# Optimization experiments

Measured on AMD Instinct MI355X. Metric: run time of the kernel, lower is better.

Reference implementation:

```python
import jax, jax.numpy as jnp
import numpy as np

KERNEL_SIZE = 5
SIGMA_INTENSITY = 0.1
SIGMA_SPATIAL = 1.0
EPS = 1e-8


def make_spatial_kernel():
    coords = jnp.arange(KERNEL_SIZE, dtype=jnp.float32) - KERNEL_SIZE // 2
    x, y = jnp.meshgrid(coords, coords, indexing='ij')
    return jnp.exp(-(x ** 2 + y ** 2) / (2.0 * SIGMA_SPATIAL ** 2))


def setup_inputs() -> dict:
    key = jax.random.key(0)
    images = jax.random.uniform(key, (16, 3, 512, 512), dtype=jnp.float32)
    spatial_kernel = make_spatial_kernel()
    return {"images": images, "spatial_kernel": spatial_kernel}


def reference(images, spatial_kernel):
    B, C, H, W = images.shape
    K = KERNEL_SIZE
    p = K // 2
    # reflect pad (torch 'reflect' == jnp 'reflect', edge not repeated)
    padded = jnp.pad(images, ((0, 0), (0, 0), (p, p), (p, p)), mode='reflect')
    # extract K*K shifted views -> (B, C, K*K, H, W); fixed small loop over offsets
    patches = jnp.stack(
        [padded[:, :, i:i + H, j:j + W] for i in range(K) for j in range(K)],
        axis=2,
    )
    center_idx = K * K // 2
    center = patches[:, :, center_idx:center_idx + 1, :, :]
    diff = patches - center
    intensity_w = jnp.exp(-(diff ** 2) / (2.0 * SIGMA_INTENSITY ** 2))
    spatial_flat = spatial_kernel.reshape(1, 1, K * K, 1, 1)
    w = spatial_flat * intensity_w
    w = w / (jnp.sum(w, axis=2, keepdims=True) + EPS)
    filtered = jnp.sum(patches * w, axis=2)  # (B, C, H, W)
    return filtered
```

## Files before the change

kernel.cpp:

```cpp
#include <hip/hip_runtime.h>

#define IMG  512
#define TW   64
#define TH   8
#define HALO 2
#define LWD  68
#define LW   69
#define LH   12

typedef float v2f __attribute__((ext_vector_type(2)));
typedef int   v2i __attribute__((ext_vector_type(2)));

#define KS2      24598.990f
#define INV_KS2  4.0652061e-05f

__device__ __forceinline__ int reflect_idx(int g) {
    int a = abs(g);
    return min(a, 2 * IMG - 2 - a);
}

__global__ __launch_bounds__(256) void bilateral_kernel(
    const float* __restrict__ img, float* __restrict__ out)
{
    __shared__ float q[LH][LW];

    const int plane = blockIdx.z;
    const int x0 = blockIdx.x * TW;
    const int y0 = blockIdx.y * TH;
    const float* __restrict__ src = img + (size_t)plane * (IMG * IMG);

    const int tid = threadIdx.x + threadIdx.y * 32;

    #pragma unroll
    for (int i = 0; i < 4; ++i) {
        int idx = tid + i * 256;
        if (idx < LH * LWD) {
            int r = idx / LWD;
            int c = idx - r * LWD;
            q[r][c] = src[reflect_idx(y0 - HALO + r) * IMG + reflect_idx(x0 - HALO + c)] * KS2;
        }
    }
    __syncthreads();

    const int tx = threadIdx.x, ty = threadIdx.y;
    const float* bp = &q[ty][2 * tx];

    v2f qc;
    qc.x = bp[2 * LW + 2];
    qc.y = bp[2 * LW + 3];

    v2f wsum = {1.0f, 1.0f};
    v2f acc  = qc;

    #pragma unroll
    for (int dy = 0; dy < 5; ++dy) {
        #pragma unroll
        for (int dx = 0; dx < 5; ++dx) {
            if (dx == 2 && dy == 2) continue;
            const int r2 = (dx - 2) * (dx - 2) + (dy - 2) * (dy - 2);
            const float Ktap = (float)(1065353216.0 - 6051101.63118 * (double)r2);

            const int off = dy * LW + dx;
            v2f qt;
            qt.x = bp[off];
            qt.y = bp[off + 1];

            v2f d = qt - qc;
            v2f t = Ktap - d * d;
            v2i iv = __builtin_convertvector(t, v2i);
            v2f e = __builtin_bit_cast(v2f, iv);

            wsum += e;
            acc  += e * qt;
        }
    }

    v2f res;
    res.x = acc.x * __builtin_amdgcn_rcpf(wsum.x) * INV_KS2;
    res.y = acc.y * __builtin_amdgcn_rcpf(wsum.y) * INV_KS2;

    float* dst = out + (size_t)plane * (IMG * IMG)
                     + (size_t)(y0 + ty) * IMG + (x0 + 2 * tx);
    *reinterpret_cast<v2f*>(dst) = res;
}

extern "C" void kernel_launch(void* const* d_in, const int* in_sizes, int n_in,
                              void* d_out, int out_size, void* d_ws, size_t ws_size,
                              hipStream_t stream) {
    const float* img = (const float*)d_in[0];
    float* out = (float*)d_out;
    int planes = in_sizes[0] / (IMG * IMG);
    dim3 grid(IMG / TW, IMG / TH, planes);
    dim3 block(32, 8, 1);
    bilateral_kernel<<<grid, block, 0, stream>>>(img, out);
}
```

Before: 131.1 us.

## Enlarge tile and compute 2x4 pixels per thread with register window

The tile grows to 128x16 and each thread now produces a 2-wide by 4-tall output patch. It loads an 8x6 window of the shared tile into registers once, so neighbouring output rows reuse those values instead of re-reading LDS for every tap. The halo load becomes row-structured, using 64-wide threads per row, which removes the per-element divide and modulo. The aim is to cut LDS traffic and halo overhead per output. The cost is more registers per thread and fewer blocks in flight.

```diff
diff --git a/kernel.cpp b/kernel.cpp
--- a/kernel.cpp
+++ b/kernel.cpp
@@ -1,12 +1,15 @@
 #include <hip/hip_runtime.h>
 
 #define IMG  512
-#define TW   64
-#define TH   8
+#define BTX  64
+#define BTY  4
+#define PXY  4
+#define TW   128
+#define TH   16
 #define HALO 2
-#define LWD  68
-#define LW   69
-#define LH   12
+#define LWD  (TW + 4)
+#define LW   136
+#define LH   (TH + 4)
 
 typedef float v2f __attribute__((ext_vector_type(2)));
 typedef int   v2i __attribute__((ext_vector_type(2)));
@@ -29,59 +32,70 @@
     const int y0 = blockIdx.y * TH;
     const float* __restrict__ src = img + (size_t)plane * (IMG * IMG);
 
-    const int tid = threadIdx.x + threadIdx.y * 32;
+    const int tx = threadIdx.x, ty = threadIdx.y;
 
     #pragma unroll
-    for (int i = 0; i < 4; ++i) {
-        int idx = tid + i * 256;
-        if (idx < LH * LWD) {
-            int r = idx / LWD;
-            int c = idx - r * LWD;
-            q[r][c] = src[reflect_idx(y0 - HALO + r) * IMG + reflect_idx(x0 - HALO + c)] * KS2;
-        }
+    for (int p = 0; p < 5; ++p) {
+        int r  = 4 * p + ty;
+        int gr = reflect_idx(y0 - HALO + r) * IMG;
+        q[r][tx]      = src[gr + reflect_idx(x0 - HALO + tx)]      * KS2;
+        q[r][tx + 64] = src[gr + reflect_idx(x0 - HALO + tx + 64)] * KS2;
+        if (tx < 4)
+            q[r][tx + 128] = src[gr + reflect_idx(x0 - HALO + tx + 128)] * KS2;
     }
     __syncthreads();
 
-    const int tx = threadIdx.x, ty = threadIdx.y;
-    const float* bp = &q[ty][2 * tx];
-
-    v2f qc;
-    qc.x = bp[2 * LW + 2];
-    qc.y = bp[2 * LW + 3];
-
-    v2f wsum = {1.0f, 1.0f};
-    v2f acc  = qc;
-
+    float w[PXY + 4][6];
     #pragma unroll
-    for (int dy = 0; dy < 5; ++dy) {
-        #pragma unroll
-        for (int dx = 0; dx < 5; ++dx) {
-            if (dx == 2 && dy == 2) continue;
-            const int r2 = (dx - 2) * (dx - 2) + (dy - 2) * (dy - 2);
-            const float Ktap = (float)(1065353216.0 - 6051101.63118 * (double)r2);
-
-            const int off = dy * LW + dx;
-            v2f qt;
-            qt.x = bp[off];
-            qt.y = bp[off + 1];
-
-            v2f d = qt - qc;
-            v2f t = Ktap - d * d;
-            v2i iv = __builtin_convertvector(t, v2i);
-            v2f e = __builtin_bit_cast(v2f, iv);
-
-            wsum += e;
-            acc  += e * qt;
-        }
+    for (int r = 0; r < PXY + 4; ++r) {
+        const float* row = &q[PXY * ty + r][2 * tx];
+        v2f a = *reinterpret_cast<const v2f*>(row);
+        v2f b = *reinterpret_cast<const v2f*>(row + 2);
+        v2f c = *reinterpret_cast<const v2f*>(row + 4);
+        w[r][0] = a.x; w[r][1] = a.y;
+        w[r][2] = b.x; w[r][3] = b.y;
+        w[r][4] = c.x; w[r][5] = c.y;
     }
 
-    v2f res;
-    res.x = acc.x * __builtin_amdgcn_rcpf(wsum.x) * INV_KS2;
-    res.y = acc.y * __builtin_amdgcn_rcpf(wsum.y) * INV_KS2;
+    v2f res[PXY];
+    #pragma unroll
+    for (int p = 0; p < PXY; ++p) {
+        v2f qc;
+        qc.x = w[p + 2][2];
+        qc.y = w[p + 2][3];
+        v2f wsum = {1.0f, 1.0f};
+        v2f acc  = qc;
+
+        #pragma unroll
+        for (int dy = 0; dy < 5; ++dy) {
+            #pragma unroll
+            for (int dx = 0; dx < 5; ++dx) {
+                if (dx == 2 && dy == 2) continue;
+                const int r2 = (dx - 2) * (dx - 2) + (dy - 2) * (dy - 2);
+                const float Ktap = (float)(1065353216.0 - 6051101.63118 * (double)r2);
+
+                v2f qt;
+                qt.x = w[p + dy][dx];
+                qt.y = w[p + dy][dx + 1];
+
+                v2f d = qt - qc;
+                v2f t = Ktap - d * d;
+                v2i iv = __builtin_convertvector(t, v2i);
+                v2f e  = __builtin_bit_cast(v2f, iv);
+
+                wsum += e;
+                acc  += e * qt;
+            }
+        }
+        res[p].x = acc.x * __builtin_amdgcn_rcpf(wsum.x) * INV_KS2;
+        res[p].y = acc.y * __builtin_amdgcn_rcpf(wsum.y) * INV_KS2;
+    }
 
     float* dst = out + (size_t)plane * (IMG * IMG)
-                     + (size_t)(y0 + ty) * IMG + (x0 + 2 * tx);
-    *reinterpret_cast<v2f*>(dst) = res;
+                     + (size_t)(y0 + PXY * ty) * IMG + (x0 + 2 * tx);
+    #pragma unroll
+    for (int p = 0; p < PXY; ++p)
+        *reinterpret_cast<v2f*>(dst + p * IMG) = res[p];
 }
 
 extern "C" void kernel_launch(void* const* d_in, const int* in_sizes, int n_in,
@@ -91,6 +105,6 @@
     float* out = (float*)d_out;
     int planes = in_sizes[0] / (IMG * IMG);
     dim3 grid(IMG / TW, IMG / TH, planes);
-    dim3 block(32, 8, 1);
+    dim3 block(BTX, BTY, 1);
     bilateral_kernel<<<grid, block, 0, stream>>>(img, out);
 }
```

Result: no change. 132.3 us (+0.9%).

## Use 64x16 tiles with row-strided per-thread outputs and scalar taps

Applied to the files above, without the earlier changes.

Reshapes the tile from 64x8 to 64x16 with 64x4 thread blocks, so each thread computes four outputs spaced four rows apart instead of two horizontally adjacent pixels. This cuts halo overhead per output and replaces the generic index-divide halo load with a row-structured load. The packed v2f math becomes scalar fmaf code. The shared tile has no padding column (LW 68), which may cause bank conflicts. The grid shrinks, so fewer blocks are available to hide latency.

```diff
diff --git a/kernel.cpp b/kernel.cpp
--- a/kernel.cpp
+++ b/kernel.cpp
@@ -1,18 +1,14 @@
 #include <hip/hip_runtime.h>
+#include <stdint.h>
 
-#define IMG  512
-#define TW   64
-#define TH   8
-#define HALO 2
-#define LWD  68
-#define LW   69
-#define LH   12
+#define IMG 512
+#define KS2     24598.990f
+#define INV_KS2 4.0652061e-05f
 
-typedef float v2f __attribute__((ext_vector_type(2)));
-typedef int   v2i __attribute__((ext_vector_type(2)));
-
-#define KS2      24598.990f
-#define INV_KS2  4.0652061e-05f
+#define TW 64
+#define TH 16
+#define LW 68
+#define LH 20
 
 __device__ __forceinline__ int reflect_idx(int g) {
     int a = abs(g);
@@ -29,59 +25,45 @@
     const int y0 = blockIdx.y * TH;
     const float* __restrict__ src = img + (size_t)plane * (IMG * IMG);
 
-    const int tid = threadIdx.x + threadIdx.y * 32;
+    const int tx = threadIdx.x, ty = threadIdx.y;
 
     #pragma unroll
-    for (int i = 0; i < 4; ++i) {
-        int idx = tid + i * 256;
-        if (idx < LH * LWD) {
-            int r = idx / LWD;
-            int c = idx - r * LWD;
-            q[r][c] = src[reflect_idx(y0 - HALO + r) * IMG + reflect_idx(x0 - HALO + c)] * KS2;
-        }
+    for (int p = 0; p < 5; ++p) {
+        int r  = ty + 4 * p;
+        int gr = reflect_idx(y0 - 2 + r) * IMG;
+        q[r][tx] = src[gr + reflect_idx(x0 - 2 + tx)] * KS2;
+        if (tx < 4)
+            q[r][tx + 64] = src[gr + reflect_idx(x0 - 2 + tx + 64)] * KS2;
     }
     __syncthreads();
 
-    const int tx = threadIdx.x, ty = threadIdx.y;
-    const float* bp = &q[ty][2 * tx];
-
-    v2f qc;
-    qc.x = bp[2 * LW + 2];
-    qc.y = bp[2 * LW + 3];
-
-    v2f wsum = {1.0f, 1.0f};
-    v2f acc  = qc;
+    float* dst = out + (size_t)plane * (IMG * IMG)
+                     + (size_t)(y0 + ty) * IMG + (x0 + tx);
 
     #pragma unroll
-    for (int dy = 0; dy < 5; ++dy) {
+    for (int k = 0; k < 4; ++k) {
+        const int row = ty + 4 * k;
+        const float qc = q[row + 2][tx + 2];
+        float wsum = 1.0f;
+        float acc  = qc;
+
         #pragma unroll
-        for (int dx = 0; dx < 5; ++dx) {
-            if (dx == 2 && dy == 2) continue;
-            const int r2 = (dx - 2) * (dx - 2) + (dy - 2) * (dy - 2);
-            const float Ktap = (float)(1065353216.0 - 6051101.63118 * (double)r2);
-
-            const int off = dy * LW + dx;
-            v2f qt;
-            qt.x = bp[off];
-            qt.y = bp[off + 1];
-
-            v2f d = qt - qc;
-            v2f t = Ktap - d * d;
-            v2i iv = __builtin_convertvector(t, v2i);
-            v2f e = __builtin_bit_cast(v2f, iv);
-
-            wsum += e;
-            acc  += e * qt;
+        for (int dy = 0; dy < 5; ++dy) {
+            #pragma unroll
+            for (int dx = 0; dx < 5; ++dx) {
+                if (dy == 2 && dx == 2) continue;
+                const int r2 = (dx - 2) * (dx - 2) + (dy - 2) * (dy - 2);
+                const float Kf = (float)(1065353216.0 - 6051101.63118 * (double)r2);
+                const float qt = q[row + dy][tx + dx];
+                const float d  = qt - qc;
+                const float t  = __builtin_fmaf(-d, d, Kf);
+                const float e  = __builtin_bit_cast(float, (int)t);
+                wsum += e;
+                acc  = __builtin_fmaf(e, qt, acc);
+            }
         }
+        dst[(size_t)(4 * k) * IMG] = acc * __builtin_amdgcn_rcpf(wsum) * INV_KS2;
     }
-
-    v2f res;
-    res.x = acc.x * __builtin_amdgcn_rcpf(wsum.x) * INV_KS2;
-    res.y = acc.y * __builtin_amdgcn_rcpf(wsum.y) * INV_KS2;
-
-    float* dst = out + (size_t)plane * (IMG * IMG)
-                     + (size_t)(y0 + ty) * IMG + (x0 + 2 * tx);
-    *reinterpret_cast<v2f*>(dst) = res;
 }
 
 extern "C" void kernel_launch(void* const* d_in, const int* in_sizes, int n_in,
@@ -89,8 +71,9 @@
                               hipStream_t stream) {
     const float* img = (const float*)d_in[0];
     float* out = (float*)d_out;
-    int planes = in_sizes[0] / (IMG * IMG);
+    const int planes = in_sizes[0] / (IMG * IMG);
+
     dim3 grid(IMG / TW, IMG / TH, planes);
-    dim3 block(32, 8, 1);
+    dim3 block(64, 4, 1);
     bilateral_kernel<<<grid, block, 0, stream>>>(img, out);
 }
```

Result: no change. 130.9 us (-0.1%).
